# Kernel tuning notes

Hardware: AMD Instinct MI355X
Metric: run time of the kernel (lower is better)

## Reference

```python
import jax, jax.numpy as jnp
import numpy as np

FLOAT_MIN = np.float32(np.finfo(np.float32).min)  # torch.finfo().min for float32
K_DIM = 64  # init kwarg, equals head dim of query/key


def setup_inputs() -> dict:
    key = jax.random.key(0)
    k1, k2, k3, k4 = jax.random.split(key, 4)
    B, Lq, Lk, D, Dv = 16, 2048, 2048, 64, 64
    return {
        "query": jax.random.normal(k1, (B, Lq, D), dtype=jnp.float32),
        "key": jax.random.normal(k2, (B, Lk, D), dtype=jnp.float32),
        "value": jax.random.normal(k3, (B, Lk, Dv), dtype=jnp.float32),
        "mask": jax.random.uniform(k4, (1, Lq, Lk), dtype=jnp.float32),
    }


def reference(query, key, value, mask):
    # scores: [B, Lq, Lk]
    scores = jnp.einsum("bqd,bkd->bqk", query, key) / jnp.sqrt(jnp.float32(K_DIM))
    # multiplicative mask -> additive log-bias, clamped at float32 min
    scores = scores + jnp.maximum(jnp.log(mask), FLOAT_MIN)
    # NOTE: source applies softmax over dim=1 (the query axis), faithfully reproduced
    attn = jax.nn.softmax(scores, axis=1)
    return jnp.einsum("bqk,bkv->bqv", attn, value)
```

## Files before the change

### kernel.cpp

```cpp
#include <hip/hip_runtime.h>
#include <cstdint>
#include <cstddef>


#define LSEQ 2048
#define DHEAD 64

typedef __bf16 v8bf __attribute__((ext_vector_type(8)));
typedef __bf16 v4bf __attribute__((ext_vector_type(4)));
typedef float v4f __attribute__((ext_vector_type(4)));

#define MFMA16(a, b, c) __builtin_amdgcn_mfma_f32_16x16x32_bf16(a, b, c, 0, 0, 0)

__device__ __forceinline__ void gl_lds16(const void* g, void* l) {
  __builtin_amdgcn_global_load_lds(
      (__attribute__((address_space(1))) void*)g,
      (__attribute__((address_space(3))) void*)l, 16, 0, 0);
}

__global__ __launch_bounds__(256) void cast_qk(const float* __restrict__ Q,
                                               const float* __restrict__ K,
                                               __bf16* __restrict__ Qb,
                                               __bf16* __restrict__ Kb) {
  size_t i = ((size_t)blockIdx.x * 256 + threadIdx.x) * 4;
  float4 q = *(const float4*)(Q + i);
  float4 k = *(const float4*)(K + i);
  v4bf qo = {(__bf16)q.x, (__bf16)q.y, (__bf16)q.z, (__bf16)q.w};
  v4bf ko = {(__bf16)k.x, (__bf16)k.y, (__bf16)k.z, (__bf16)k.w};
  *(v4bf*)(Qb + i) = qo;
  *(v4bf*)(Kb + i) = ko;
}

__global__ __launch_bounds__(256) void stats_k(const __bf16* __restrict__ Qb,
                                               const __bf16* __restrict__ Kb,
                                               const float* __restrict__ mask,
                                               float* __restrict__ Lsum) {
  const int bx = blockIdx.x;
  const int b = bx >> 7;
  const int qc = (bx >> 5) & 3;
  const int k0 = (bx & 31) * 64;
  const int tid = threadIdx.x;
  const int wave = tid >> 6, lane = tid & 63;
  const int quad = lane >> 4, n = lane & 15;

  __shared__ __align__(16) __bf16 Qt[64 * 64];
  __shared__ float psum[4][64];

  v8bf bk[4][2];
#pragma unroll
  for (int sub = 0; sub < 4; ++sub)
#pragma unroll
    for (int dh = 0; dh < 2; ++dh)
      bk[sub][dh] = *(const v8bf*)(Kb + ((size_t)b * LSEQ + k0 + sub * 16 + n) * DHEAD +
                                   dh * 32 + quad * 8);

  float colsum[4] = {0.f, 0.f, 0.f, 0.f};

  const int qbeg = qc * 512;
  for (int q0 = qbeg; q0 < qbeg + 512; q0 += 64) {
    __syncthreads();
#pragma unroll
    for (int i = 0; i < 2; ++i) {
      int s = (wave * 2 + i) * 64 + lane;
      int row = s >> 3, gc = (s & 7) ^ (row & 7);
      gl_lds16(Qb + ((size_t)b * LSEQ + q0 + row) * DHEAD + gc * 8, &Qt[s * 8]);
    }
    __syncthreads();

    v8bf aq[2];
    const int qr = wave * 16 + n;
#pragma unroll
    for (int dh = 0; dh < 2; ++dh)
      aq[dh] = *(const v8bf*)&Qt[qr * 64 + ((dh * 4 + quad) ^ (qr & 7)) * 8];

#pragma unroll
    for (int sub = 0; sub < 4; ++sub) {
      v4f c = {0.f, 0.f, 0.f, 0.f};
      c = MFMA16(aq[0], bk[sub][0], c);
      c = MFMA16(aq[1], bk[sub][1], c);
      const int kg = k0 + sub * 16 + n;
#pragma unroll
      for (int r = 0; r < 4; ++r) {
        int qg = q0 + wave * 16 + quad * 4 + r;
        float p = mask[(size_t)qg * LSEQ + kg] * __expf(c[r] * 0.125f);
        colsum[sub] += p;
      }
    }
  }

#pragma unroll
  for (int sub = 0; sub < 4; ++sub) {
    float v = colsum[sub];
    v += __shfl_xor(v, 16);
    v += __shfl_xor(v, 32);
    if (quad == 0) psum[wave][sub * 16 + n] = v;
  }
  __syncthreads();
  if (tid < 64) {
    float s = psum[0][tid] + psum[1][tid] + psum[2][tid] + psum[3][tid];
    unsafeAtomicAdd(&Lsum[(size_t)b * LSEQ + k0 + tid], s);
  }
}

__global__ __launch_bounds__(256) void vtrans_k(const float* __restrict__ V,
                                                const float* __restrict__ Lsum,
                                                __bf16* __restrict__ Vts) {
  const int b = blockIdx.x >> 6;
  const int k0 = (blockIdx.x & 63) * 32;
  const int tid = threadIdx.x;
  __shared__ float tile[32][65];
  __shared__ float invl[32];
  if (tid < 32) invl[tid] = 1.0f / Lsum[(size_t)b * LSEQ + k0 + tid];
#pragma unroll
  for (int t = 0; t < 8; ++t) {
    int flat = t * 256 + tid;
    int k = flat >> 6, v = flat & 63;
    tile[k][v] = V[((size_t)b * LSEQ + k0 + k) * DHEAD + v];
  }
  __syncthreads();
#pragma unroll
  for (int t = 0; t < 8; ++t) {
    int flat = t * 256 + tid;
    int v = flat >> 5, k = flat & 31;
    Vts[((size_t)b * DHEAD + v) * LSEQ + k0 + k] = (__bf16)(tile[k][v] * invl[k]);
  }
}

__global__ __launch_bounds__(256) void attn_k(const __bf16* __restrict__ Qb,
                                              const __bf16* __restrict__ Kb,
                                              const __bf16* __restrict__ Vts,
                                              const float* __restrict__ mask,
                                              float* __restrict__ out) {
  const int bx = blockIdx.x;
  const int b = bx >> 7;
  const int kc = (bx >> 5) & 3;
  const int q0 = (bx & 31) * 64;
  const int tid = threadIdx.x;
  const int wave = tid >> 6, lane = tid & 63;
  const int quad = lane >> 4, n = lane & 15;

  __shared__ __align__(16) __bf16 Kt[64 * 64];
  __shared__ __align__(16) __bf16 Vt[64 * 64];
  __shared__ __align__(16) __bf16 Pt[64 * 72];

  v8bf aq[2];
  {
    const int qr = q0 + wave * 16 + n;
#pragma unroll
    for (int dh = 0; dh < 2; ++dh)
      aq[dh] = *(const v8bf*)(Qb + ((size_t)b * LSEQ + qr) * DHEAD + dh * 32 + quad * 8);
  }

  v4f acc[4];
#pragma unroll
  for (int vs = 0; vs < 4; ++vs) acc[vs] = (v4f){0.f, 0.f, 0.f, 0.f};

  const int kbeg = kc * 512;
  for (int k0 = kbeg; k0 < kbeg + 512; k0 += 64) {
    __syncthreads();
#pragma unroll
    for (int i = 0; i < 2; ++i) {
      int s = (wave * 2 + i) * 64 + lane;
      int row = s >> 3, gc = (s & 7) ^ (row & 7);
      gl_lds16(Kb + ((size_t)b * LSEQ + k0 + row) * DHEAD + gc * 8, &Kt[s * 8]);
      gl_lds16(Vts + ((size_t)b * DHEAD + row) * LSEQ + k0 + gc * 8, &Vt[s * 8]);
    }
    __syncthreads();

#pragma unroll
    for (int sub = 0; sub < 4; ++sub) {
      v4f c = {0.f, 0.f, 0.f, 0.f};
      const int kr = sub * 16 + n;
#pragma unroll
      for (int dh = 0; dh < 2; ++dh) {
        v8bf bkf = *(const v8bf*)&Kt[kr * 64 + ((dh * 4 + quad) ^ (kr & 7)) * 8];
        c = MFMA16(aq[dh], bkf, c);
      }
      const int kg = k0 + kr;
#pragma unroll
      for (int r = 0; r < 4; ++r) {
        int qg = q0 + wave * 16 + quad * 4 + r;
        float p = mask[(size_t)qg * LSEQ + kg] * __expf(c[r] * 0.125f);
        Pt[(wave * 16 + quad * 4 + r) * 72 + kr] = (__bf16)p;
      }
    }
    __asm__ volatile("s_waitcnt lgkmcnt(0)" ::: "memory");

#pragma unroll
    for (int kk = 0; kk < 2; ++kk) {
      v8bf ap = *(const v8bf*)&Pt[(wave * 16 + n) * 72 + kk * 32 + quad * 8];
#pragma unroll
      for (int vs = 0; vs < 4; ++vs) {
        const int vr = vs * 16 + n;
        v8bf bv = *(const v8bf*)&Vt[vr * 64 + ((kk * 4 + quad) ^ (vr & 7)) * 8];
        acc[vs] = MFMA16(ap, bv, acc[vs]);
      }
    }
  }

#pragma unroll
  for (int vs = 0; vs < 4; ++vs)
#pragma unroll
    for (int r = 0; r < 4; ++r)
      unsafeAtomicAdd(
          &out[((size_t)b * LSEQ + q0 + wave * 16 + quad * 4 + r) * DHEAD + vs * 16 + n],
          acc[vs][r]);
}

extern "C" void kernel_launch(void* const* d_in, const int* in_sizes, int n_in,
                              void* d_out, int out_size, void* d_ws, size_t ws_size,
                              hipStream_t stream) {
  const float* Q = (const float*)d_in[0];
  const float* K = (const float*)d_in[1];
  const float* V = (const float*)d_in[2];
  const float* mask = (const float*)d_in[3];
  float* out = (float*)d_out;

  char* ws = (char*)d_ws;
  __bf16* Qb = (__bf16*)(ws);
  __bf16* Kb = (__bf16*)(ws + 4194304);
  __bf16* Vts = (__bf16*)(ws + 8388608);
  float* Lsum = (float*)(ws + 12582912);
  if (ws_size < 12713984) return;

  hipMemsetAsync(Lsum, 0, LSEQ * 16 * sizeof(float), stream);
  hipMemsetAsync(out, 0, (size_t)out_size * sizeof(float), stream);
  cast_qk<<<2048, 256, 0, stream>>>(Q, K, Qb, Kb);
  stats_k<<<2048, 256, 0, stream>>>(Qb, Kb, mask, Lsum);
  vtrans_k<<<1024, 256, 0, stream>>>(V, Lsum, Vts);
  attn_k<<<2048, 256, 0, stream>>>(Qb, Kb, Vts, mask, out);
}
```

Before: 171.3 us.

## Materialize P once in stats pass and replace recompute with streaming PV GEMM

The column-stats kernel now also writes the unnormalized bf16 probability matrix P to a workspace buffer, so the attention kernel no longer recomputes QK^T, exp and the mask multiply. It becomes a plain P·V GEMM that streams P from global memory. Work is processed in batch groups sized to fit the workspace. The 1/sqrt(d) scale is folded into the Q cast, and the output and Lsum zeroing are fused into the cast kernel in place of the memsets. The trade is 8 MB of P writes and reads per batch instead of a second pass over the mask and recomputed scores, and PV loads now bypass LDS.

```diff
diff --git a/kernel.cpp b/kernel.cpp
--- a/kernel.cpp
+++ b/kernel.cpp
@@ -12,38 +12,42 @@
 
 #define MFMA16(a, b, c) __builtin_amdgcn_mfma_f32_16x16x32_bf16(a, b, c, 0, 0, 0)
 
-__device__ __forceinline__ void gl_lds16(const void* g, void* l) {
-  __builtin_amdgcn_global_load_lds(
-      (__attribute__((address_space(1))) void*)g,
-      (__attribute__((address_space(3))) void*)l, 16, 0, 0);
-}
-
 __global__ __launch_bounds__(256) void cast_qk(const float* __restrict__ Q,
                                                const float* __restrict__ K,
                                                __bf16* __restrict__ Qb,
-                                               __bf16* __restrict__ Kb) {
-  size_t i = ((size_t)blockIdx.x * 256 + threadIdx.x) * 4;
+                                               __bf16* __restrict__ Kb,
+                                               float* __restrict__ outz,
+                                               float* __restrict__ Lz) {
+  size_t j = (size_t)blockIdx.x * 256 + threadIdx.x;
+  size_t i = j * 4;
   float4 q = *(const float4*)(Q + i);
   float4 k = *(const float4*)(K + i);
-  v4bf qo = {(__bf16)q.x, (__bf16)q.y, (__bf16)q.z, (__bf16)q.w};
+  v4bf qo = {(__bf16)(q.x * 0.125f), (__bf16)(q.y * 0.125f),
+             (__bf16)(q.z * 0.125f), (__bf16)(q.w * 0.125f)};
   v4bf ko = {(__bf16)k.x, (__bf16)k.y, (__bf16)k.z, (__bf16)k.w};
   *(v4bf*)(Qb + i) = qo;
   *(v4bf*)(Kb + i) = ko;
-}
-
-__global__ __launch_bounds__(256) void stats_k(const __bf16* __restrict__ Qb,
-                                               const __bf16* __restrict__ Kb,
-                                               const float* __restrict__ mask,
-                                               float* __restrict__ Lsum) {
+  float4 z = {0.f, 0.f, 0.f, 0.f};
+  *(float4*)(outz + i) = z;
+  if (j < (size_t)16 * LSEQ) Lz[j] = 0.f;
+}
+
+__global__ __launch_bounds__(256) void prod_k(const __bf16* __restrict__ Qb,
+                                              const __bf16* __restrict__ Kb,
+                                              const float* __restrict__ mask,
+                                              float* __restrict__ Lsum,
+                                              __bf16* __restrict__ Pg,
+                                              int b0) {
   const int bx = blockIdx.x;
-  const int b = bx >> 7;
+  const int bl = bx >> 7;
+  const int b = b0 + bl;
   const int qc = (bx >> 5) & 3;
   const int k0 = (bx & 31) * 64;
   const int tid = threadIdx.x;
-  const int wave = tid >> 6, lane = tid & 63;
+  const int w = tid >> 6, lane = tid & 63;
   const int quad = lane >> 4, n = lane & 15;
 
-  __shared__ __align__(16) __bf16 Qt[64 * 64];
+  __shared__ __align__(16) __bf16 Pt[64 * 64];
   __shared__ float psum[4][64];
 
   v8bf bk[4][2];
@@ -55,37 +59,52 @@
                                    dh * 32 + quad * 8);
 
   float colsum[4] = {0.f, 0.f, 0.f, 0.f};
-
-  const int qbeg = qc * 512;
-  for (int q0 = qbeg; q0 < qbeg + 512; q0 += 64) {
-    __syncthreads();
-#pragma unroll
-    for (int i = 0; i < 2; ++i) {
-      int s = (wave * 2 + i) * 64 + lane;
-      int row = s >> 3, gc = (s & 7) ^ (row & 7);
-      gl_lds16(Qb + ((size_t)b * LSEQ + q0 + row) * DHEAD + gc * 8, &Qt[s * 8]);
-    }
-    __syncthreads();
-
-    v8bf aq[2];
-    const int qr = wave * 16 + n;
-#pragma unroll
-    for (int dh = 0; dh < 2; ++dh)
-      aq[dh] = *(const v8bf*)&Qt[qr * 64 + ((dh * 4 + quad) ^ (qr & 7)) * 8];
+  const int rrow = w * 16 + (lane >> 2);
+  const int c4 = lane & 3;
+
+  const int qbeg = qc * 512, qend = qbeg + 512;
+  v8bf aq[2];
+  {
+    const size_t qgr = (size_t)b * LSEQ + qbeg + w * 16 + n;
+    aq[0] = *(const v8bf*)(Qb + qgr * DHEAD + quad * 8);
+    aq[1] = *(const v8bf*)(Qb + qgr * DHEAD + 32 + quad * 8);
+  }
+#pragma unroll 1
+  for (int q0 = qbeg; q0 < qend; q0 += 64) {
+    const int qn = (q0 + 64 < qend) ? q0 + 64 : qbeg;
+    v8bf nq0, nq1;
+    {
+      const size_t qgr = (size_t)b * LSEQ + qn + w * 16 + n;
+      nq0 = *(const v8bf*)(Qb + qgr * DHEAD + quad * 8);
+      nq1 = *(const v8bf*)(Qb + qgr * DHEAD + 32 + quad * 8);
+    }
 
 #pragma unroll
     for (int sub = 0; sub < 4; ++sub) {
       v4f c = {0.f, 0.f, 0.f, 0.f};
       c = MFMA16(aq[0], bk[sub][0], c);
       c = MFMA16(aq[1], bk[sub][1], c);
-      const int kg = k0 + sub * 16 + n;
+      const int kr = sub * 16 + n;
+      const int kg = k0 + kr;
 #pragma unroll
       for (int r = 0; r < 4; ++r) {
-        int qg = q0 + wave * 16 + quad * 4 + r;
-        float p = mask[(size_t)qg * LSEQ + kg] * __expf(c[r] * 0.125f);
+        const int qrow = w * 16 + quad * 4 + r;
+        float p = mask[(size_t)(q0 + qrow) * LSEQ + kg] * __expf(c[r]);
         colsum[sub] += p;
+        Pt[qrow * 64 + ((((kr >> 3)) ^ (qrow & 7)) << 3) + (kr & 7)] = (__bf16)p;
       }
     }
+
+#pragma unroll
+    for (int p2 = 0; p2 < 2; ++p2) {
+      const int phys = c4 + 4 * ((rrow + p2) & 1);
+      const int logi = phys ^ (rrow & 7);
+      v8bf v = *(const v8bf*)&Pt[rrow * 64 + phys * 8];
+      *(v8bf*)(Pg + ((size_t)bl * LSEQ + q0 + rrow) * LSEQ + k0 + logi * 8) = v;
+    }
+
+    aq[0] = nq0;
+    aq[1] = nq1;
   }
 
 #pragma unroll
@@ -93,7 +112,7 @@
     float v = colsum[sub];
     v += __shfl_xor(v, 16);
     v += __shfl_xor(v, 32);
-    if (quad == 0) psum[wave][sub * 16 + n] = v;
+    if (quad == 0) psum[w][sub * 16 + n] = v;
   }
   __syncthreads();
   if (tid < 64) {
@@ -104,8 +123,8 @@
 
 __global__ __launch_bounds__(256) void vtrans_k(const float* __restrict__ V,
                                                 const float* __restrict__ Lsum,
-                                                __bf16* __restrict__ Vts) {
-  const int b = blockIdx.x >> 6;
+                                                __bf16* __restrict__ Vts, int b0) {
+  const int b = b0 + (blockIdx.x >> 6);
   const int k0 = (blockIdx.x & 63) * 32;
   const int tid = threadIdx.x;
   __shared__ float tile[32][65];
@@ -126,75 +145,36 @@
   }
 }
 
-__global__ __launch_bounds__(256) void attn_k(const __bf16* __restrict__ Qb,
-                                              const __bf16* __restrict__ Kb,
-                                              const __bf16* __restrict__ Vts,
-                                              const float* __restrict__ mask,
-                                              float* __restrict__ out) {
+__global__ __launch_bounds__(256) void pv_k(const __bf16* __restrict__ Pg,
+                                            const __bf16* __restrict__ Vts,
+                                            float* __restrict__ out,
+                                            int b0, int bgm, int bgs) {
   const int bx = blockIdx.x;
-  const int b = bx >> 7;
-  const int kc = (bx >> 5) & 3;
-  const int q0 = (bx & 31) * 64;
+  const int bl = bx & bgm;
+  const int rest = bx >> bgs;
+  const int kc = rest & 1;
+  const int qt = rest >> 1;
+  const int b = b0 + bl;
+  const int q0 = qt * 64;
   const int tid = threadIdx.x;
-  const int wave = tid >> 6, lane = tid & 63;
+  const int w = tid >> 6, lane = tid & 63;
   const int quad = lane >> 4, n = lane & 15;
 
-  __shared__ __align__(16) __bf16 Kt[64 * 64];
-  __shared__ __align__(16) __bf16 Vt[64 * 64];
-  __shared__ __align__(16) __bf16 Pt[64 * 72];
-
-  v8bf aq[2];
-  {
-    const int qr = q0 + wave * 16 + n;
-#pragma unroll
-    for (int dh = 0; dh < 2; ++dh)
-      aq[dh] = *(const v8bf*)(Qb + ((size_t)b * LSEQ + qr) * DHEAD + dh * 32 + quad * 8);
-  }
+  const __bf16* pbase =
+      Pg + ((size_t)bl * LSEQ + q0 + w * 16 + n) * LSEQ + kc * 1024 + quad * 8;
+  const __bf16* vbase = Vts + ((size_t)b * DHEAD + n) * LSEQ + kc * 1024 + quad * 8;
 
   v4f acc[4];
 #pragma unroll
   for (int vs = 0; vs < 4; ++vs) acc[vs] = (v4f){0.f, 0.f, 0.f, 0.f};
 
-  const int kbeg = kc * 512;
-  for (int k0 = kbeg; k0 < kbeg + 512; k0 += 64) {
-    __syncthreads();
-#pragma unroll
-    for (int i = 0; i < 2; ++i) {
-      int s = (wave * 2 + i) * 64 + lane;
-      int row = s >> 3, gc = (s & 7) ^ (row & 7);
-      gl_lds16(Kb + ((size_t)b * LSEQ + k0 + row) * DHEAD + gc * 8, &Kt[s * 8]);
-      gl_lds16(Vts + ((size_t)b * DHEAD + row) * LSEQ + k0 + gc * 8, &Vt[s * 8]);
-    }
-    __syncthreads();
-
-#pragma unroll
-    for (int sub = 0; sub < 4; ++sub) {
-      v4f c = {0.f, 0.f, 0.f, 0.f};
-      const int kr = sub * 16 + n;
-#pragma unroll
-      for (int dh = 0; dh < 2; ++dh) {
-        v8bf bkf = *(const v8bf*)&Kt[kr * 64 + ((dh * 4 + quad) ^ (kr & 7)) * 8];
-        c = MFMA16(aq[dh], bkf, c);
-      }
-      const int kg = k0 + kr;
-#pragma unroll
-      for (int r = 0; r < 4; ++r) {
-        int qg = q0 + wave * 16 + quad * 4 + r;
-        float p = mask[(size_t)qg * LSEQ + kg] * __expf(c[r] * 0.125f);
-        Pt[(wave * 16 + quad * 4 + r) * 72 + kr] = (__bf16)p;
-      }
-    }
-    __asm__ volatile("s_waitcnt lgkmcnt(0)" ::: "memory");
-
-#pragma unroll
-    for (int kk = 0; kk < 2; ++kk) {
-      v8bf ap = *(const v8bf*)&Pt[(wave * 16 + n) * 72 + kk * 32 + quad * 8];
-#pragma unroll
-      for (int vs = 0; vs < 4; ++vs) {
-        const int vr = vs * 16 + n;
-        v8bf bv = *(const v8bf*)&Vt[vr * 64 + ((kk * 4 + quad) ^ (vr & 7)) * 8];
-        acc[vs] = MFMA16(ap, bv, acc[vs]);
-      }
+#pragma unroll 4
+  for (int i = 0; i < 32; ++i) {
+    v8bf ap = *(const v8bf*)(pbase + i * 32);
+#pragma unroll
+    for (int vs = 0; vs < 4; ++vs) {
+      v8bf bv = *(const v8bf*)(vbase + (size_t)vs * 16 * LSEQ + i * 32);
+      acc[vs] = MFMA16(ap, bv, acc[vs]);
     }
   }
 
@@ -203,7 +183,7 @@
 #pragma unroll
     for (int r = 0; r < 4; ++r)
       unsafeAtomicAdd(
-          &out[((size_t)b * LSEQ + q0 + wave * 16 + quad * 4 + r) * DHEAD + vs * 16 + n],
+          &out[((size_t)b * LSEQ + q0 + w * 16 + quad * 4 + r) * DHEAD + vs * 16 + n],
           acc[vs][r]);
 }
 
@@ -218,15 +198,24 @@
 
   char* ws = (char*)d_ws;
   __bf16* Qb = (__bf16*)(ws);
-  __bf16* Kb = (__bf16*)(ws + 4194304);
-  __bf16* Vts = (__bf16*)(ws + 8388608);
-  float* Lsum = (float*)(ws + 12582912);
-  if (ws_size < 12713984) return;
-
-  hipMemsetAsync(Lsum, 0, LSEQ * 16 * sizeof(float), stream);
-  hipMemsetAsync(out, 0, (size_t)out_size * sizeof(float), stream);
-  cast_qk<<<2048, 256, 0, stream>>>(Q, K, Qb, Kb);
-  stats_k<<<2048, 256, 0, stream>>>(Qb, Kb, mask, Lsum);
-  vtrans_k<<<1024, 256, 0, stream>>>(V, Lsum, Vts);
-  attn_k<<<2048, 256, 0, stream>>>(Qb, Kb, Vts, mask, out);
-}
+  __bf16* Kb = (__bf16*)(ws + (4 << 20));
+  __bf16* Vts = (__bf16*)(ws + (8 << 20));
+  float* Lsum = (float*)(ws + (12 << 20));
+  __bf16* Pg = (__bf16*)(ws + (12 << 20) + (1 << 17));
+  const size_t base = ((size_t)12 << 20) + (1 << 17);
+  const size_t perb = (size_t)LSEQ * LSEQ * 2;
+  if (ws_size < base + perb) return;
+
+  int bg = (int)((ws_size - base) / perb);
+  if (bg > 16) bg = 16;
+  while (bg & (bg - 1)) bg &= bg - 1;
+  int bgs = 0;
+  while ((1 << (bgs + 1)) <= bg) ++bgs;
+
+  cast_qk<<<2048, 256, 0, stream>>>(Q, K, Qb, Kb, out, Lsum);
+  for (int g = 0; g < 16; g += bg) {
+    prod_k<<<bg * 128, 256, 0, stream>>>(Qb, Kb, mask, Lsum, Pg, g);
+    vtrans_k<<<bg * 64, 256, 0, stream>>>(V, Lsum, Vts, g);
+    pv_k<<<bg * 64, 256, 0, stream>>>(Pg, Vts, out, g, bg - 1, bgs);
+  }
+}
```

After: 210.0 us. 22.6% more time.

## Transpose mask once, fold scale into Q, register-prefetch operands without LDS

Applied to the files above, without the earlier changes.

A fused prep kernel casts Q (pre-scaled by 1/8) and K to bf16, zeroes the output and the column-sum buffer in place of the memsets, and writes a transposed copy of the mask. The stats kernel then reads the mask as contiguous float4 vectors and double-buffers Q and mask loads in registers instead of staging through LDS. The attention kernel swaps MFMA operand roles so each lane reads contiguous mask vectors, loads K and V fragments directly from global memory with a one-step prefetch, and uses LDS only for P. This trades an extra full-mask transpose pass and more registers for coalesced mask reads and fewer barriers.

```diff
diff --git a/kernel.cpp b/kernel.cpp
--- a/kernel.cpp
+++ b/kernel.cpp
@@ -12,38 +12,65 @@
 
 #define MFMA16(a, b, c) __builtin_amdgcn_mfma_f32_16x16x32_bf16(a, b, c, 0, 0, 0)
 
-__device__ __forceinline__ void gl_lds16(const void* g, void* l) {
-  __builtin_amdgcn_global_load_lds(
-      (__attribute__((address_space(1))) void*)g,
-      (__attribute__((address_space(3))) void*)l, 16, 0, 0);
-}
-
-__global__ __launch_bounds__(256) void cast_qk(const float* __restrict__ Q,
-                                               const float* __restrict__ K,
-                                               __bf16* __restrict__ Qb,
-                                               __bf16* __restrict__ Kb) {
-  size_t i = ((size_t)blockIdx.x * 256 + threadIdx.x) * 4;
-  float4 q = *(const float4*)(Q + i);
-  float4 k = *(const float4*)(K + i);
-  v4bf qo = {(__bf16)q.x, (__bf16)q.y, (__bf16)q.z, (__bf16)q.w};
-  v4bf ko = {(__bf16)k.x, (__bf16)k.y, (__bf16)k.z, (__bf16)k.w};
-  *(v4bf*)(Qb + i) = qo;
-  *(v4bf*)(Kb + i) = ko;
-}
-
-__global__ __launch_bounds__(256) void stats_k(const __bf16* __restrict__ Qb,
-                                               const __bf16* __restrict__ Kb,
-                                               const float* __restrict__ mask,
-                                               float* __restrict__ Lsum) {
+__global__ __launch_bounds__(256) void prep_k(const float* __restrict__ Q,
+                                              const float* __restrict__ K,
+                                              const float* __restrict__ mask,
+                                              __bf16* __restrict__ Qb,
+                                              __bf16* __restrict__ Kb,
+                                              float* __restrict__ maskT,
+                                              float* __restrict__ outz,
+                                              float* __restrict__ Lz) {
+  const int bx = blockIdx.x;
+  const int tid = threadIdx.x;
+  if (bx < 2048) {
+    size_t j = (size_t)bx * 256 + tid;
+    size_t i = j * 4;
+    float4 q = *(const float4*)(Q + i);
+    float4 k = *(const float4*)(K + i);
+    v4bf qo = {(__bf16)(q.x * 0.125f), (__bf16)(q.y * 0.125f),
+               (__bf16)(q.z * 0.125f), (__bf16)(q.w * 0.125f)};
+    v4bf ko = {(__bf16)k.x, (__bf16)k.y, (__bf16)k.z, (__bf16)k.w};
+    *(v4bf*)(Qb + i) = qo;
+    *(v4bf*)(Kb + i) = ko;
+    float4 z = {0.f, 0.f, 0.f, 0.f};
+    *(float4*)(outz + i) = z;
+    if (j < (size_t)16 * LSEQ) Lz[j] = 0.f;
+  } else {
+    __shared__ __align__(16) float tile[64][68];
+    const int t = bx - 2048;
+    const int q0t = (t & 31) * 64;
+    const int k0t = (t >> 5) * 64;
+#pragma unroll
+    for (int p = 0; p < 4; ++p) {
+      int flat = p * 1024 + tid * 4;
+      int r = flat >> 6, c = flat & 63;
+      float4 v = *(const float4*)(mask + (size_t)(q0t + r) * LSEQ + k0t + c);
+      *(float4*)&tile[r][c] = v;
+    }
+    __syncthreads();
+#pragma unroll
+    for (int p = 0; p < 4; ++p) {
+      int flat = p * 1024 + tid * 4;
+      int kr = flat >> 6, qc2 = flat & 63;
+      float4 o = {tile[qc2][kr], tile[qc2 + 1][kr], tile[qc2 + 2][kr],
+                  tile[qc2 + 3][kr]};
+      *(float4*)(maskT + (size_t)(k0t + kr) * LSEQ + q0t + qc2) = o;
+    }
+  }
+}
+
+__global__ __launch_bounds__(256, 4) void stats_k(const __bf16* __restrict__ Qb,
+                                                  const __bf16* __restrict__ Kb,
+                                                  const float* __restrict__ maskT,
+                                                  float* __restrict__ Lsum) {
   const int bx = blockIdx.x;
   const int b = bx >> 7;
   const int qc = (bx >> 5) & 3;
   const int k0 = (bx & 31) * 64;
   const int tid = threadIdx.x;
-  const int wave = tid >> 6, lane = tid & 63;
+  const int w = tid >> 6, lane = tid & 63;
   const int quad = lane >> 4, n = lane & 15;
 
-  __shared__ __align__(16) __bf16 Qt[64 * 64];
   __shared__ float psum[4][64];
 
   v8bf bk[4][2];
@@ -55,37 +82,43 @@
                                    dh * 32 + quad * 8);
 
   float colsum[4] = {0.f, 0.f, 0.f, 0.f};
-
   const int qbeg = qc * 512;
-  for (int q0 = qbeg; q0 < qbeg + 512; q0 += 64) {
-    __syncthreads();
-#pragma unroll
-    for (int i = 0; i < 2; ++i) {
-      int s = (wave * 2 + i) * 64 + lane;
-      int row = s >> 3, gc = (s & 7) ^ (row & 7);
-      gl_lds16(Qb + ((size_t)b * LSEQ + q0 + row) * DHEAD + gc * 8, &Qt[s * 8]);
-    }
-    __syncthreads();
-
-    v8bf aq[2];
-    const int qr = wave * 16 + n;
-#pragma unroll
-    for (int dh = 0; dh < 2; ++dh)
-      aq[dh] = *(const v8bf*)&Qt[qr * 64 + ((dh * 4 + quad) ^ (qr & 7)) * 8];
-
+
+  v8bf aq0, aq1, nq0, nq1;
+  float4 m4[4], nm[4];
+  {
+    const __bf16* qp = Qb + ((size_t)b * LSEQ + qbeg + w * 16 + n) * DHEAD + quad * 8;
+    aq0 = *(const v8bf*)qp;
+    aq1 = *(const v8bf*)(qp + 32);
+#pragma unroll
+    for (int sub = 0; sub < 4; ++sub)
+      m4[sub] = *(const float4*)(maskT + (size_t)(k0 + sub * 16 + n) * LSEQ + qbeg +
+                                 w * 16 + quad * 4);
+  }
+#pragma unroll 1
+  for (int ks = 0; ks < 8; ++ks) {
+    const int qnext = qbeg + ((ks + 1) & 7) * 64;
+    {
+      const __bf16* qp = Qb + ((size_t)b * LSEQ + qnext + w * 16 + n) * DHEAD + quad * 8;
+      nq0 = *(const v8bf*)qp;
+      nq1 = *(const v8bf*)(qp + 32);
+#pragma unroll
+      for (int sub = 0; sub < 4; ++sub)
+        nm[sub] = *(const float4*)(maskT + (size_t)(k0 + sub * 16 + n) * LSEQ + qnext +
+                                   w * 16 + quad * 4);
+    }
 #pragma unroll
     for (int sub = 0; sub < 4; ++sub) {
       v4f c = {0.f, 0.f, 0.f, 0.f};
-      c = MFMA16(aq[0], bk[sub][0], c);
-      c = MFMA16(aq[1], bk[sub][1], c);
-      const int kg = k0 + sub * 16 + n;
-#pragma unroll
-      for (int r = 0; r < 4; ++r) {
-        int qg = q0 + wave * 16 + quad * 4 + r;
-        float p = mask[(size_t)qg * LSEQ + kg] * __expf(c[r] * 0.125f);
-        colsum[sub] += p;
-      }
-    }
+      c = MFMA16(aq0, bk[sub][0], c);
+      c = MFMA16(aq1, bk[sub][1], c);
+      colsum[sub] += m4[sub].x * __expf(c[0]) + m4[sub].y * __expf(c[1]) +
+                     m4[sub].z * __expf(c[2]) + m4[sub].w * __expf(c[3]);
+    }
+    aq0 = nq0;
+    aq1 = nq1;
+#pragma unroll
+    for (int sub = 0; sub < 4; ++sub) m4[sub] = nm[sub];
   }
 
 #pragma unroll
@@ -93,7 +126,7 @@
     float v = colsum[sub];
     v += __shfl_xor(v, 16);
     v += __shfl_xor(v, 32);
-    if (quad == 0) psum[wave][sub * 16 + n] = v;
+    if (quad == 0) psum[w][sub * 16 + n] = v;
   }
   __syncthreads();
   if (tid < 64) {
@@ -126,85 +159,88 @@
   }
 }
 
-__global__ __launch_bounds__(256) void attn_k(const __bf16* __restrict__ Qb,
-                                              const __bf16* __restrict__ Kb,
-                                              const __bf16* __restrict__ Vts,
-                                              const float* __restrict__ mask,
-                                              float* __restrict__ out) {
+__global__ __launch_bounds__(256, 3) void attn_k(const __bf16* __restrict__ Qb,
+                                                 const __bf16* __restrict__ Kb,
+                                                 const __bf16* __restrict__ Vts,
+                                                 const float* __restrict__ mask,
+                                                 float* __restrict__ out) {
   const int bx = blockIdx.x;
   const int b = bx >> 7;
   const int kc = (bx >> 5) & 3;
   const int q0 = (bx & 31) * 64;
   const int tid = threadIdx.x;
-  const int wave = tid >> 6, lane = tid & 63;
+  const int w = tid >> 6, lane = tid & 63;
   const int quad = lane >> 4, n = lane & 15;
 
-  __shared__ __align__(16) __bf16 Kt[64 * 64];
-  __shared__ __align__(16) __bf16 Vt[64 * 64];
-  __shared__ __align__(16) __bf16 Pt[64 * 72];
-
-  v8bf aq[2];
-  {
-    const int qr = q0 + wave * 16 + n;
-#pragma unroll
-    for (int dh = 0; dh < 2; ++dh)
-      aq[dh] = *(const v8bf*)(Qb + ((size_t)b * LSEQ + qr) * DHEAD + dh * 32 + quad * 8);
-  }
+  __shared__ __align__(16) __bf16 Pt[64][72];
+
+  const int qg = q0 + w * 16 + n;
+
+  v8bf bq[2];
+#pragma unroll
+  for (int dh = 0; dh < 2; ++dh)
+    bq[dh] = *(const v8bf*)(Qb + ((size_t)b * LSEQ + qg) * DHEAD + dh * 32 + quad * 8);
 
   v4f acc[4];
 #pragma unroll
   for (int vs = 0; vs < 4; ++vs) acc[vs] = (v4f){0.f, 0.f, 0.f, 0.f};
 
   const int kbeg = kc * 512;
-  for (int k0 = kbeg; k0 < kbeg + 512; k0 += 64) {
-    __syncthreads();
-#pragma unroll
-    for (int i = 0; i < 2; ++i) {
-      int s = (wave * 2 + i) * 64 + lane;
-      int row = s >> 3, gc = (s & 7) ^ (row & 7);
-      gl_lds16(Kb + ((size_t)b * LSEQ + k0 + row) * DHEAD + gc * 8, &Kt[s * 8]);
-      gl_lds16(Vts + ((size_t)b * DHEAD + row) * LSEQ + k0 + gc * 8, &Vt[s * 8]);
-    }
-    __syncthreads();
-
+  const __bf16* kbase = Kb + (size_t)b * LSEQ * DHEAD;
+  const float* mbase = mask + (size_t)qg * LSEQ;
+
+  v8bf ak[4][2];
+  float4 m4[4];
+#define LOAD_STEP(kb)                                                                  \
+  {                                                                                    \
+    _Pragma("unroll") for (int sub = 0; sub < 4; ++sub) {                              \
+      _Pragma("unroll") for (int dh = 0; dh < 2; ++dh) ak[sub][dh] =                   \
+          *(const v8bf*)(kbase + (size_t)((kb) + sub * 16 + n) * DHEAD + dh * 32 +     \
+                         quad * 8);                                                    \
+      m4[sub] = *(const float4*)(mbase + (kb) + sub * 16 + quad * 4);                  \
+    }                                                                                  \
+  }
+  LOAD_STEP(kbeg);
+
+#pragma unroll 1
+  for (int ks = 0; ks < 8; ++ks) {
+    const int kb = kbeg + ks * 64;
 #pragma unroll
     for (int sub = 0; sub < 4; ++sub) {
       v4f c = {0.f, 0.f, 0.f, 0.f};
-      const int kr = sub * 16 + n;
-#pragma unroll
-      for (int dh = 0; dh < 2; ++dh) {
-        v8bf bkf = *(const v8bf*)&Kt[kr * 64 + ((dh * 4 + quad) ^ (kr & 7)) * 8];
-        c = MFMA16(aq[dh], bkf, c);
-      }
-      const int kg = k0 + kr;
-#pragma unroll
-      for (int r = 0; r < 4; ++r) {
-        int qg = q0 + wave * 16 + quad * 4 + r;
-        float p = mask[(size_t)qg * LSEQ + kg] * __expf(c[r] * 0.125f);
-        Pt[(wave * 16 + quad * 4 + r) * 72 + kr] = (__bf16)p;
-      }
-    }
+      c = MFMA16(ak[sub][0], bq[0], c);
+      c = MFMA16(ak[sub][1], bq[1], c);
+      v4bf pv;
+      pv[0] = (__bf16)(m4[sub].x * __expf(c[0]));
+      pv[1] = (__bf16)(m4[sub].y * __expf(c[1]));
+      pv[2] = (__bf16)(m4[sub].z * __expf(c[2]));
+      pv[3] = (__bf16)(m4[sub].w * __expf(c[3]));
+      *(v4bf*)&Pt[w * 16 + n][sub * 16 + quad * 4] = pv;
+    }
+    v8bf av[4][2];
+#pragma unroll
+    for (int vs = 0; vs < 4; ++vs)
+#pragma unroll
+      for (int kk = 0; kk < 2; ++kk)
+        av[vs][kk] = *(const v8bf*)(Vts + ((size_t)b * DHEAD + vs * 16 + n) * LSEQ + kb +
+                                    kk * 32 + quad * 8);
+    if (ks < 7) LOAD_STEP(kb + 64);
     __asm__ volatile("s_waitcnt lgkmcnt(0)" ::: "memory");
-
 #pragma unroll
     for (int kk = 0; kk < 2; ++kk) {
-      v8bf ap = *(const v8bf*)&Pt[(wave * 16 + n) * 72 + kk * 32 + quad * 8];
-#pragma unroll
-      for (int vs = 0; vs < 4; ++vs) {
-        const int vr = vs * 16 + n;
-        v8bf bv = *(const v8bf*)&Vt[vr * 64 + ((kk * 4 + quad) ^ (vr & 7)) * 8];
-        acc[vs] = MFMA16(ap, bv, acc[vs]);
-      }
-    }
-  }
-
+      v8bf pb = *(const v8bf*)&Pt[w * 16 + n][kk * 32 + quad * 8];
+#pragma unroll
+      for (int vs = 0; vs < 4; ++vs) acc[vs] = MFMA16(av[vs][kk], pb, acc[vs]);
+    }
+  }
+#undef LOAD_STEP
+
+  float* obase = out + ((size_t)b * LSEQ + qg) * DHEAD;
 #pragma unroll
   for (int vs = 0; vs < 4; ++vs)
 #pragma unroll
     for (int r = 0; r < 4; ++r)
-      unsafeAtomicAdd(
-          &out[((size_t)b * LSEQ + q0 + wave * 16 + quad * 4 + r) * DHEAD + vs * 16 + n],
-          acc[vs][r]);
+      unsafeAtomicAdd(obase + vs * 16 + quad * 4 + r, acc[vs][r]);
 }
 
 extern "C" void kernel_launch(void* const* d_in, const int* in_sizes, int n_in,
@@ -218,15 +254,15 @@
 
   char* ws = (char*)d_ws;
   __bf16* Qb = (__bf16*)(ws);
-  __bf16* Kb = (__bf16*)(ws + 4194304);
-  __bf16* Vts = (__bf16*)(ws + 8388608);
-  float* Lsum = (float*)(ws + 12582912);
-  if (ws_size < 12713984) return;
-
-  hipMemsetAsync(Lsum, 0, LSEQ * 16 * sizeof(float), stream);
-  hipMemsetAsync(out, 0, (size_t)out_size * sizeof(float), stream);
-  cast_qk<<<2048, 256, 0, stream>>>(Q, K, Qb, Kb);
-  stats_k<<<2048, 256, 0, stream>>>(Qb, Kb, mask, Lsum);
+  __bf16* Kb = (__bf16*)(ws + (4 << 20));
+  __bf16* Vts = (__bf16*)(ws + (8 << 20));
+  float* Lsum = (float*)(ws + (12 << 20));
+  float* maskT = (float*)(ws + (12 << 20) + (1 << 17));
+  const size_t need = ((size_t)12 << 20) + (1 << 17) + (size_t)LSEQ * LSEQ * 4;
+  if (ws_size < need) return;
+
+  prep_k<<<3072, 256, 0, stream>>>(Q, K, mask, Qb, Kb, maskT, out, Lsum);
+  stats_k<<<2048, 256, 0, stream>>>(Qb, Kb, maskT, Lsum);
   vtrans_k<<<1024, 256, 0, stream>>>(V, Lsum, Vts);
   attn_k<<<2048, 256, 0, stream>>>(Qb, Kb, Vts, mask, out);
 }
```

New measurement: 331.5 us. 93.5% more time.

## Double-buffer LDS tiles, prefetch mask, fold memsets and scale into cast

Applied to the files above, without the earlier changes.

The stats and attention kernels now double-buffer their Q and K/V LDS tiles and prefetch the next mask tile into registers, which overlaps global loads with MFMA/exp work and halves the barriers per iteration. The MFMA operand order is swapped so each lane holds four consecutive key columns, allowing vectorized float4 mask loads and v4bf P stores. The 1/8 scale is folded into the Q cast, and zeroing of out and Lsum moves into the cast kernel, replacing two memset calls. Occupancy hints are added through launch_bounds, which raises register pressure from the prefetch buffers.

```diff
diff --git a/kernel.cpp b/kernel.cpp
--- a/kernel.cpp
+++ b/kernel.cpp
@@ -21,80 +21,116 @@
 __global__ __launch_bounds__(256) void cast_qk(const float* __restrict__ Q,
                                                const float* __restrict__ K,
                                                __bf16* __restrict__ Qb,
-                                               __bf16* __restrict__ Kb) {
-  size_t i = ((size_t)blockIdx.x * 256 + threadIdx.x) * 4;
+                                               __bf16* __restrict__ Kb,
+                                               float* __restrict__ outz,
+                                               float* __restrict__ Lz) {
+  size_t j = (size_t)blockIdx.x * 256 + threadIdx.x;
+  size_t i = j * 4;
   float4 q = *(const float4*)(Q + i);
   float4 k = *(const float4*)(K + i);
-  v4bf qo = {(__bf16)q.x, (__bf16)q.y, (__bf16)q.z, (__bf16)q.w};
+  v4bf qo = {(__bf16)(q.x * 0.125f), (__bf16)(q.y * 0.125f),
+             (__bf16)(q.z * 0.125f), (__bf16)(q.w * 0.125f)};
   v4bf ko = {(__bf16)k.x, (__bf16)k.y, (__bf16)k.z, (__bf16)k.w};
   *(v4bf*)(Qb + i) = qo;
   *(v4bf*)(Kb + i) = ko;
-}
-
-__global__ __launch_bounds__(256) void stats_k(const __bf16* __restrict__ Qb,
-                                               const __bf16* __restrict__ Kb,
-                                               const float* __restrict__ mask,
-                                               float* __restrict__ Lsum) {
+  float4 z = {0.f, 0.f, 0.f, 0.f};
+  *(float4*)(outz + i) = z;
+  if (j < (size_t)16 * LSEQ) Lz[j] = 0.f;
+}
+
+__global__ __launch_bounds__(256, 4) void stats_k(const __bf16* __restrict__ Qb,
+                                                  const __bf16* __restrict__ Kb,
+                                                  const float* __restrict__ mask,
+                                                  float* __restrict__ Lsum) {
   const int bx = blockIdx.x;
   const int b = bx >> 7;
   const int qc = (bx >> 5) & 3;
   const int k0 = (bx & 31) * 64;
   const int tid = threadIdx.x;
-  const int wave = tid >> 6, lane = tid & 63;
+  const int w = tid >> 6, lane = tid & 63;
   const int quad = lane >> 4, n = lane & 15;
 
-  __shared__ __align__(16) __bf16 Qt[64 * 64];
+  __shared__ __align__(16) __bf16 Qt[2][64 * 64];
   __shared__ float psum[4][64];
 
-  v8bf bk[4][2];
+#define STAGE_Q(buf, q0s)                                                        \
+  {                                                                              \
+    _Pragma("unroll") for (int i = 0; i < 2; ++i) {                              \
+      int s = (w * 2 + i) * 64 + lane;                                           \
+      int row = s >> 3, gc = (s & 7) ^ (row & 7);                                \
+      gl_lds16(Qb + ((size_t)b * LSEQ + (q0s) + row) * DHEAD + gc * 8,           \
+               &Qt[buf][s * 8]);                                                 \
+    }                                                                            \
+  }
+
+  v8bf ak[4][2];
 #pragma unroll
   for (int sub = 0; sub < 4; ++sub)
 #pragma unroll
     for (int dh = 0; dh < 2; ++dh)
-      bk[sub][dh] = *(const v8bf*)(Kb + ((size_t)b * LSEQ + k0 + sub * 16 + n) * DHEAD +
+      ak[sub][dh] = *(const v8bf*)(Kb + ((size_t)b * LSEQ + k0 + sub * 16 + n) * DHEAD +
                                    dh * 32 + quad * 8);
 
-  float colsum[4] = {0.f, 0.f, 0.f, 0.f};
+  float csum[4][4];
+#pragma unroll
+  for (int sub = 0; sub < 4; ++sub)
+#pragma unroll
+    for (int r = 0; r < 4; ++r) csum[sub][r] = 0.f;
 
   const int qbeg = qc * 512;
-  for (int q0 = qbeg; q0 < qbeg + 512; q0 += 64) {
-    __syncthreads();
-#pragma unroll
-    for (int i = 0; i < 2; ++i) {
-      int s = (wave * 2 + i) * 64 + lane;
-      int row = s >> 3, gc = (s & 7) ^ (row & 7);
-      gl_lds16(Qb + ((size_t)b * LSEQ + q0 + row) * DHEAD + gc * 8, &Qt[s * 8]);
-    }
-    __syncthreads();
-
-    v8bf aq[2];
-    const int qr = wave * 16 + n;
+  STAGE_Q(0, qbeg);
+  v4f m4[4], nm[4];
+#pragma unroll
+  for (int sub = 0; sub < 4; ++sub)
+    m4[sub] = *(const v4f*)(mask + (size_t)(qbeg + w * 16 + n) * LSEQ + k0 + sub * 16 +
+                            quad * 4);
+  __syncthreads();
+
+  int cur = 0;
+#pragma unroll 1
+  for (int ks = 0; ks < 8; ++ks) {
+    const int qs = qbeg + ks * 64;
+    if (ks < 7) {
+      STAGE_Q(cur ^ 1, qs + 64);
+#pragma unroll
+      for (int sub = 0; sub < 4; ++sub)
+        nm[sub] = *(const v4f*)(mask + (size_t)(qs + 64 + w * 16 + n) * LSEQ + k0 +
+                                sub * 16 + quad * 4);
+    }
+    const int qr = w * 16 + n;
+    v8bf bq[2];
 #pragma unroll
     for (int dh = 0; dh < 2; ++dh)
-      aq[dh] = *(const v8bf*)&Qt[qr * 64 + ((dh * 4 + quad) ^ (qr & 7)) * 8];
+      bq[dh] = *(const v8bf*)&Qt[cur][qr * 64 + ((dh * 4 + quad) ^ (qr & 7)) * 8];
 
 #pragma unroll
     for (int sub = 0; sub < 4; ++sub) {
       v4f c = {0.f, 0.f, 0.f, 0.f};
-      c = MFMA16(aq[0], bk[sub][0], c);
-      c = MFMA16(aq[1], bk[sub][1], c);
-      const int kg = k0 + sub * 16 + n;
-#pragma unroll
-      for (int r = 0; r < 4; ++r) {
-        int qg = q0 + wave * 16 + quad * 4 + r;
-        float p = mask[(size_t)qg * LSEQ + kg] * __expf(c[r] * 0.125f);
-        colsum[sub] += p;
-      }
-    }
-  }
-
-#pragma unroll
-  for (int sub = 0; sub < 4; ++sub) {
-    float v = colsum[sub];
-    v += __shfl_xor(v, 16);
-    v += __shfl_xor(v, 32);
-    if (quad == 0) psum[wave][sub * 16 + n] = v;
-  }
+      c = MFMA16(ak[sub][0], bq[0], c);
+      c = MFMA16(ak[sub][1], bq[1], c);
+#pragma unroll
+      for (int r = 0; r < 4; ++r) csum[sub][r] += m4[sub][r] * __expf(c[r]);
+    }
+    __syncthreads();
+    if (ks < 7) {
+#pragma unroll
+      for (int sub = 0; sub < 4; ++sub) m4[sub] = nm[sub];
+    }
+    cur ^= 1;
+  }
+#undef STAGE_Q
+
+#pragma unroll
+  for (int sub = 0; sub < 4; ++sub)
+#pragma unroll
+    for (int r = 0; r < 4; ++r) {
+      float v = csum[sub][r];
+      v += __shfl_xor(v, 1);
+      v += __shfl_xor(v, 2);
+      v += __shfl_xor(v, 4);
+      v += __shfl_xor(v, 8);
+      if (n == 0) psum[w][sub * 16 + quad * 4 + r] = v;
+    }
   __syncthreads();
   if (tid < 64) {
     float s = psum[0][tid] + psum[1][tid] + psum[2][tid] + psum[3][tid];
@@ -126,84 +162,106 @@
   }
 }
 
-__global__ __launch_bounds__(256) void attn_k(const __bf16* __restrict__ Qb,
-                                              const __bf16* __restrict__ Kb,
-                                              const __bf16* __restrict__ Vts,
-                                              const float* __restrict__ mask,
-                                              float* __restrict__ out) {
+__global__ __launch_bounds__(256, 3) void attn_k(const __bf16* __restrict__ Qb,
+                                                 const __bf16* __restrict__ Kb,
+                                                 const __bf16* __restrict__ Vts,
+                                                 const float* __restrict__ mask,
+                                                 float* __restrict__ out) {
   const int bx = blockIdx.x;
   const int b = bx >> 7;
   const int kc = (bx >> 5) & 3;
   const int q0 = (bx & 31) * 64;
   const int tid = threadIdx.x;
-  const int wave = tid >> 6, lane = tid & 63;
+  const int w = tid >> 6, lane = tid & 63;
   const int quad = lane >> 4, n = lane & 15;
 
-  __shared__ __align__(16) __bf16 Kt[64 * 64];
-  __shared__ __align__(16) __bf16 Vt[64 * 64];
-  __shared__ __align__(16) __bf16 Pt[64 * 72];
-
-  v8bf aq[2];
-  {
-    const int qr = q0 + wave * 16 + n;
-#pragma unroll
-    for (int dh = 0; dh < 2; ++dh)
-      aq[dh] = *(const v8bf*)(Qb + ((size_t)b * LSEQ + qr) * DHEAD + dh * 32 + quad * 8);
-  }
+  __shared__ __align__(16) __bf16 Kt[2][64 * 64];
+  __shared__ __align__(16) __bf16 Vt[2][64 * 64];
+  __shared__ __align__(16) __bf16 Pt[64][72];
+
+#define STAGE_KV(buf, kb2)                                                       \
+  {                                                                              \
+    _Pragma("unroll") for (int i = 0; i < 2; ++i) {                              \
+      int s = (w * 2 + i) * 64 + lane;                                           \
+      int row = s >> 3, gc = (s & 7) ^ (row & 7);                                \
+      gl_lds16(Kb + ((size_t)b * LSEQ + (kb2) + row) * DHEAD + gc * 8,           \
+               &Kt[buf][s * 8]);                                                 \
+      gl_lds16(Vts + ((size_t)b * DHEAD + row) * LSEQ + (kb2) + gc * 8,          \
+               &Vt[buf][s * 8]);                                                 \
+    }                                                                            \
+  }
+
+  const int qg = q0 + w * 16 + n;
+
+  v8bf bq[2];
+#pragma unroll
+  for (int dh = 0; dh < 2; ++dh)
+    bq[dh] = *(const v8bf*)(Qb + ((size_t)b * LSEQ + qg) * DHEAD + dh * 32 + quad * 8);
 
   v4f acc[4];
 #pragma unroll
   for (int vs = 0; vs < 4; ++vs) acc[vs] = (v4f){0.f, 0.f, 0.f, 0.f};
 
   const int kbeg = kc * 512;
-  for (int k0 = kbeg; k0 < kbeg + 512; k0 += 64) {
-    __syncthreads();
-#pragma unroll
-    for (int i = 0; i < 2; ++i) {
-      int s = (wave * 2 + i) * 64 + lane;
-      int row = s >> 3, gc = (s & 7) ^ (row & 7);
-      gl_lds16(Kb + ((size_t)b * LSEQ + k0 + row) * DHEAD + gc * 8, &Kt[s * 8]);
-      gl_lds16(Vts + ((size_t)b * DHEAD + row) * LSEQ + k0 + gc * 8, &Vt[s * 8]);
-    }
-    __syncthreads();
+  STAGE_KV(0, kbeg);
+  v4f m4[4], nm[4];
+#pragma unroll
+  for (int sub = 0; sub < 4; ++sub)
+    m4[sub] = *(const v4f*)(mask + (size_t)qg * LSEQ + kbeg + sub * 16 + quad * 4);
+  __syncthreads();
+
+  int cur = 0;
+#pragma unroll 1
+  for (int ks = 0; ks < 8; ++ks) {
+    const int kb = kbeg + ks * 64;
+    if (ks < 7) {
+      STAGE_KV(cur ^ 1, kb + 64);
+#pragma unroll
+      for (int sub = 0; sub < 4; ++sub)
+        nm[sub] =
+            *(const v4f*)(mask + (size_t)qg * LSEQ + kb + 64 + sub * 16 + quad * 4);
+    }
 
 #pragma unroll
     for (int sub = 0; sub < 4; ++sub) {
+      const int kr = sub * 16 + n;
+      v8bf a0 = *(const v8bf*)&Kt[cur][kr * 64 + ((quad) ^ (kr & 7)) * 8];
+      v8bf a1 = *(const v8bf*)&Kt[cur][kr * 64 + ((4 + quad) ^ (kr & 7)) * 8];
       v4f c = {0.f, 0.f, 0.f, 0.f};
-      const int kr = sub * 16 + n;
-#pragma unroll
-      for (int dh = 0; dh < 2; ++dh) {
-        v8bf bkf = *(const v8bf*)&Kt[kr * 64 + ((dh * 4 + quad) ^ (kr & 7)) * 8];
-        c = MFMA16(aq[dh], bkf, c);
-      }
-      const int kg = k0 + kr;
-#pragma unroll
-      for (int r = 0; r < 4; ++r) {
-        int qg = q0 + wave * 16 + quad * 4 + r;
-        float p = mask[(size_t)qg * LSEQ + kg] * __expf(c[r] * 0.125f);
-        Pt[(wave * 16 + quad * 4 + r) * 72 + kr] = (__bf16)p;
-      }
+      c = MFMA16(a0, bq[0], c);
+      c = MFMA16(a1, bq[1], c);
+      v4bf pv;
+#pragma unroll
+      for (int r = 0; r < 4; ++r) pv[r] = (__bf16)(m4[sub][r] * __expf(c[r]));
+      *(v4bf*)&Pt[w * 16 + n][sub * 16 + quad * 4] = pv;
     }
     __asm__ volatile("s_waitcnt lgkmcnt(0)" ::: "memory");
 
 #pragma unroll
     for (int kk = 0; kk < 2; ++kk) {
-      v8bf ap = *(const v8bf*)&Pt[(wave * 16 + n) * 72 + kk * 32 + quad * 8];
+      v8bf ap = *(const v8bf*)&Pt[w * 16 + n][kk * 32 + quad * 8];
 #pragma unroll
       for (int vs = 0; vs < 4; ++vs) {
         const int vr = vs * 16 + n;
-        v8bf bv = *(const v8bf*)&Vt[vr * 64 + ((kk * 4 + quad) ^ (vr & 7)) * 8];
+        v8bf bv = *(const v8bf*)&Vt[cur][vr * 64 + ((kk * 4 + quad) ^ (vr & 7)) * 8];
         acc[vs] = MFMA16(ap, bv, acc[vs]);
       }
     }
-  }
+    __syncthreads();
+    if (ks < 7) {
+#pragma unroll
+      for (int sub = 0; sub < 4; ++sub) m4[sub] = nm[sub];
+    }
+    cur ^= 1;
+  }
+#undef STAGE_KV
 
 #pragma unroll
   for (int vs = 0; vs < 4; ++vs)
 #pragma unroll
     for (int r = 0; r < 4; ++r)
       unsafeAtomicAdd(
-          &out[((size_t)b * LSEQ + q0 + wave * 16 + quad * 4 + r) * DHEAD + vs * 16 + n],
+          &out[((size_t)b * LSEQ + q0 + w * 16 + quad * 4 + r) * DHEAD + vs * 16 + n],
           acc[vs][r]);
 }
 
@@ -218,14 +276,13 @@
 
   char* ws = (char*)d_ws;
   __bf16* Qb = (__bf16*)(ws);
-  __bf16* Kb = (__bf16*)(ws + 4194304);
-  __bf16* Vts = (__bf16*)(ws + 8388608);
-  float* Lsum = (float*)(ws + 12582912);
-  if (ws_size < 12713984) return;
-
-  hipMemsetAsync(Lsum, 0, LSEQ * 16 * sizeof(float), stream);
-  hipMemsetAsync(out, 0, (size_t)out_size * sizeof(float), stream);
-  cast_qk<<<2048, 256, 0, stream>>>(Q, K, Qb, Kb);
+  __bf16* Kb = (__bf16*)(ws + (4 << 20));
+  __bf16* Vts = (__bf16*)(ws + (8 << 20));
+  float* Lsum = (float*)(ws + (12 << 20));
+  const size_t need = ((size_t)12 << 20) + (1 << 17);
+  if (ws_size < need) return;
+
+  cast_qk<<<2048, 256, 0, stream>>>(Q, K, Qb, Kb, out, Lsum);
   stats_k<<<2048, 256, 0, stream>>>(Qb, Kb, mask, Lsum);
   vtrans_k<<<1024, 256, 0, stream>>>(V, Lsum, Vts);
   attn_k<<<2048, 256, 0, stream>>>(Qb, Kb, Vts, mask, out);
```

New measurement: 189.5 us. +10.6%, slower.
